# Optimization experiments

Measured on AMD Instinct MI355X. Metric: run time of the kernel, lower is better.

Reference implementation:

```python
import jax, jax.numpy as jnp
import numpy as np

LN_EPS = 1e-5
ROPE_BASE = 10000.0


def rotate_half(x):
    # x: [..., d]; split into two halves (matches einops '(j d)->j d', j=2)
    d2 = x.shape[-1] // 2
    x1, x2 = x[..., :d2], x[..., d2:]
    return jnp.concatenate((-x2, x1), axis=-1)


def rotary_pos_emb(n, head_dim, dtype=jnp.float32):
    inv_freq = 1.0 / (ROPE_BASE ** (jnp.arange(0, head_dim, 2, dtype=jnp.float32) / head_dim))
    t = jnp.arange(n, dtype=jnp.float32)
    freqs = jnp.einsum('i,j->ij', t, inv_freq)          # [n, d/2]
    return jnp.concatenate((freqs, freqs), axis=-1).astype(dtype)  # [n, d]


def apply_rotary(pos, t):
    return t * jnp.cos(pos) + rotate_half(t) * jnp.sin(pos)


def setup_inputs() -> dict:
    key = jax.random.key(0)
    ks = jax.random.split(key, 4)
    b, n, dm = 2, 4096, 2048
    x = jax.random.normal(ks[0], (b, n, dm), dtype=jnp.float32)
    wq = jax.random.normal(ks[1], (dm, dm), dtype=jnp.float32) * (dm ** -0.5)
    wk = jax.random.normal(ks[2], (dm, dm), dtype=jnp.float32) * (dm ** -0.5)
    wv = jax.random.normal(ks[3], (dm, dm), dtype=jnp.float32) * (dm ** -0.5)
    return {
        'x': x,
        'ln_gamma': jnp.ones((dm,), jnp.float32),
        'ln_beta': jnp.zeros((dm,), jnp.float32),
        'wq': wq, 'wk': wk, 'wv': wv,
        'num_heads': 16,
    }


def reference(x, ln_gamma, ln_beta, wq, wk, wv, num_heads):
    b, n, dm = x.shape
    hd = dm // num_heads
    # LayerNorm (eps=1e-5, torch default)
    mu = jnp.mean(x, axis=-1, keepdims=True)
    var = jnp.mean(jnp.square(x - mu), axis=-1, keepdims=True)
    xn = (x - mu) * jax.lax.rsqrt(var + LN_EPS) * ln_gamma + ln_beta
    # QKV projections (nn.Linear, bias=False => x @ W.T; weights stored as [out,in])
    q = jnp.einsum('bnd,ed->bne', xn, wq)
    k = jnp.einsum('bnd,ed->bne', xn, wk)
    v = jnp.einsum('bnd,ed->bne', xn, wv)
    # b n (h d) -> b h n d
    split = lambda t: t.reshape(b, n, num_heads, hd).transpose(0, 2, 1, 3)
    q, k, v = split(q), split(k), split(v)
    pos = rotary_pos_emb(n, hd, x.dtype)  # [n, hd], broadcasts over b,h
    q = apply_rotary(pos, q)
    k = apply_rotary(pos, k)
    return q, k, v
```

## Files before the change

### kernel.cpp

```cpp
#include <hip/hip_runtime.h>
#include <hip/hip_bf16.h>


typedef float f32x4 __attribute__((ext_vector_type(4)));
typedef __bf16 bf16x8 __attribute__((ext_vector_type(8)));
typedef __bf16 bf16x4 __attribute__((ext_vector_type(4)));

#define DM    2048
#define NSEQ  4096
#define NH    16
#define HD    128
#define NROWS 8192
#define MAT_ELEMS (2ull*NH*NSEQ*HD)

typedef __attribute__((address_space(1))) const void GV;
typedef __attribute__((address_space(3))) void LV;
__device__ __forceinline__ void gload_lds16(const void* g, void* l) {
    __builtin_amdgcn_global_load_lds((GV*)g, (LV*)l, 16, 0, 0);
}

__global__ __launch_bounds__(256)
void ln_kernel(const float* __restrict__ x, const float* __restrict__ g,
               const float* __restrict__ be, __bf16* __restrict__ xnb) {
    int row = blockIdx.x;
    int tid = threadIdx.x;
    const float4* xr = (const float4*)(x + (size_t)row * DM);
    float4 v0 = xr[tid];
    float4 v1 = xr[tid + 256];
    float s  = v0.x + v0.y + v0.z + v0.w + v1.x + v1.y + v1.z + v1.w;
    float ss = v0.x*v0.x + v0.y*v0.y + v0.z*v0.z + v0.w*v0.w
             + v1.x*v1.x + v1.y*v1.y + v1.z*v1.z + v1.w*v1.w;
#pragma unroll
    for (int o = 32; o > 0; o >>= 1) {
        s  += __shfl_down(s, o);
        ss += __shfl_down(ss, o);
    }
    __shared__ float red[10];
    int wave = tid >> 6, lane = tid & 63;
    if (lane == 0) { red[wave] = s; red[4 + wave] = ss; }
    __syncthreads();
    if (tid == 0) {
        float S  = red[0] + red[1] + red[2] + red[3];
        float SS = red[4] + red[5] + red[6] + red[7];
        float mu  = S * (1.0f / DM);
        float var = SS * (1.0f / DM) - mu * mu;
        red[8] = mu;
        red[9] = rsqrtf(var + 1e-5f);
    }
    __syncthreads();
    float mu = red[8], rs = red[9];

    const float4* gp = (const float4*)g;
    const float4* bp = (const float4*)be;
    bf16x4* orow = (bf16x4*)(xnb + (size_t)row * DM);
    {
        float4 g0 = gp[tid], b0 = bp[tid];
        bf16x4 o;
        o[0] = (__bf16)((v0.x - mu) * rs * g0.x + b0.x);
        o[1] = (__bf16)((v0.y - mu) * rs * g0.y + b0.y);
        o[2] = (__bf16)((v0.z - mu) * rs * g0.z + b0.z);
        o[3] = (__bf16)((v0.w - mu) * rs * g0.w + b0.w);
        orow[tid] = o;
    }
    {
        float4 g1 = gp[tid + 256], b1 = bp[tid + 256];
        bf16x4 o;
        o[0] = (__bf16)((v1.x - mu) * rs * g1.x + b1.x);
        o[1] = (__bf16)((v1.y - mu) * rs * g1.y + b1.y);
        o[2] = (__bf16)((v1.z - mu) * rs * g1.z + b1.z);
        o[3] = (__bf16)((v1.w - mu) * rs * g1.w + b1.w);
        orow[tid + 256] = o;
    }
}

__global__ __launch_bounds__(256)
void cvt3_kernel(const float* __restrict__ a0, const float* __restrict__ a1,
                 const float* __restrict__ a2, __bf16* __restrict__ o) {
    int bid = blockIdx.x;
    const float* a = (bid < 2048) ? a0 : (bid < 4096) ? a1 : a2;
    size_t base = ((size_t)(bid & 2047) * 256 + threadIdx.x) * 8;
    float4 v0 = *(const float4*)(a + base);
    float4 v1 = *(const float4*)(a + base + 4);
    bf16x8 r;
    r[0] = (__bf16)v0.x; r[1] = (__bf16)v0.y; r[2] = (__bf16)v0.z; r[3] = (__bf16)v0.w;
    r[4] = (__bf16)v1.x; r[5] = (__bf16)v1.y; r[6] = (__bf16)v1.z; r[7] = (__bf16)v1.w;
    *(bf16x8*)(o + (size_t)(bid >> 11) * 4194304 + base) = r;
}


__device__ __forceinline__ void loadA(bf16x8 (&a)[4], const __bf16* Sp,
                                      int base, int oo) {
#pragma unroll
    for (int mi = 0; mi < 4; mi++)
        a[mi] = *(const bf16x8*)(Sp + base + mi * 1024 + oo);
}
__device__ __forceinline__ void loadB(bf16x8 (&b)[4], const __bf16* Sp,
                                      int base, int oo) {
#pragma unroll
    for (int j = 0; j < 4; j++)
        b[j] = *(const bf16x8*)(Sp + base + (j * 16 + (j >> 1) * 32) * 64 + oo);
}

template<int RB>
__device__ __forceinline__ void cluster(f32x4 (&acc)[8][4], bf16x8 (&a)[4],
                                        bf16x8 (&b)[4]) {
    __builtin_amdgcn_s_setprio(1);
#pragma unroll
    for (int mi = 0; mi < 4; mi++)
#pragma unroll
        for (int ni = 0; ni < 4; ni++)
            acc[RB + mi][ni] = __builtin_amdgcn_mfma_f32_16x16x32_bf16(
                a[mi], b[ni], acc[RB + mi][ni], 0, 0, 0);
    __builtin_amdgcn_s_setprio(0);
}

#define FENCE asm volatile("" ::: "memory")
#define BAR   do { FENCE; __builtin_amdgcn_s_barrier(); FENCE; } while (0)
#define VM8   asm volatile("s_waitcnt vmcnt(8)" ::: "memory")
#define VM6   asm volatile("s_waitcnt vmcnt(6)" ::: "memory")
#define VM2   asm volatile("s_waitcnt vmcnt(2)" ::: "memory")
#define VM0   asm volatile("s_waitcnt vmcnt(0)" ::: "memory")
#define VMX   do {} while (0)

#define STGA(P, kt, HF) do { \
    gload_lds16(pA + (size_t)((HF) * 64 + w * 8) * DM + (kt) * 64,       &As[P][((HF) * 8 + w) * 512]); \
    gload_lds16(pA + (size_t)((HF) * 64 + 128 + w * 8) * DM + (kt) * 64, &As[P][((HF) * 8 + 16 + w) * 512]); \
} while (0)
#define STGB(P, kt, HF) do { \
    gload_lds16(pB + (size_t)((HF) * 64 + w * 8) * DM + (kt) * 64,       &Bs[P][((HF) * 8 + w) * 512]); \
    gload_lds16(pB + (size_t)((HF) * 64 + 128 + w * 8) * DM + (kt) * 64, &Bs[P][((HF) * 8 + 16 + w) * 512]); \
} while (0)

#define KTILE(kt, P, Q, SG0, SG2, SG3, W0, W2) do { \
     \
    loadA(a0, &As[P][0], baseA, o0); \
    loadB(b0, &Bs[P][0], baseB, o0); \
    if (SG0) STGA(Q, (kt) + 1, 1); \
    W0; BAR; cluster<0>(acc, a0, b0); BAR; \
     \
    loadA(a1, &As[P][0], baseA, o1); \
    loadB(b1, &Bs[P][0], baseB, o1); \
    BAR; cluster<0>(acc, a1, b1); BAR; \
     \
    loadA(a0, &As[P][0], baseA + 4096, o0); \
    if (SG2) { STGA(P, (kt) + 2, 0); STGB(P, (kt) + 2, 0); } \
    W2; BAR; cluster<4>(acc, a0, b0); BAR; \
     \
    loadA(a1, &As[P][0], baseA + 4096, o1); \
    if (SG3) STGB(P, (kt) + 2, 1); \
    BAR; cluster<4>(acc, a1, b1); BAR; \
} while (0)

__global__ __launch_bounds__(512, 2)
void gemm_qkv(const __bf16* __restrict__ A,
              const __bf16* __restrict__ Wq,
              const __bf16* __restrict__ Wk,
              const __bf16* __restrict__ Wv,
              float* __restrict__ out) {
    __shared__ __bf16 As[2][16384];
    __shared__ __bf16 Bs[2][16384];

    int tid = threadIdx.x;
    int w = tid >> 6, l = tid & 63;
    int wm = w >> 2, wn = w & 3;

    int bid = blockIdx.x;
    int x = bid & 7;
    int ridx = bid >> 3;
    int q = ridx >> 5;
    int s = ridx & 31;
    int mtp, ntp;
    if (q == 0)      { mtp = s >> 3;       ntp = s & 7; }
    else if (q == 1) { mtp = 4 + (s >> 3); ntp = s & 7; }
    else             { mtp = s & 7;        ntp = 8 + (s >> 3); }
    int mt = (x & 3) * 8 + mtp;
    int nt = (x >> 2) * 12 + ntp;
    int mat = nt >> 3, ntb = nt & 7;
    const __bf16* Wp = (mat == 0) ? Wq : (mat == 1) ? Wk : Wv;
    int row0 = mt * 256, colp = ntb * 256;

    int lr = l >> 3;
    int lco = ((l & 7) ^ lr) * 8;
    const __bf16* pA = A  + (size_t)(row0 + lr) * DM + lco;
    const __bf16* pB = Wp + (size_t)(colp + lr) * DM + lco;

    int baseA = (wm * 128 + (l & 15)) * 64;
    int baseB = ((wn & 1) * 32 + (wn >> 1) * 128 + (l & 15)) * 64;
    int o0 = ((l >> 4) * 8) ^ ((l & 7) * 8);
    int o1 = o0 ^ 32;

    STGA(0, 0, 0); STGB(0, 0, 0); STGB(0, 0, 1); STGA(0, 0, 1);
    STGA(1, 1, 0); STGB(1, 1, 0); STGB(1, 1, 1);

    f32x4 acc[8][4];
#pragma unroll
    for (int i = 0; i < 8; i++)
#pragma unroll
        for (int j = 0; j < 4; j++)
            acc[i][j] = (f32x4){0.f, 0.f, 0.f, 0.f};

    bf16x8 a0[4], a1[4], b0[4], b1[4];

    VM8;
    BAR;

#pragma unroll 1
    for (int kt = 0; kt < 30; kt += 2) {
        KTILE(kt,     0, 1, 1, 1, 1, VM8, VM6);
        KTILE(kt + 1, 1, 0, 1, 1, 1, VM8, VM6);
    }
    KTILE(30, 0, 1, 1, 0, 0, VM8, VM2);
    KTILE(31, 1, 0, 0, 0, 0, VM0, VMX);

    float* op = out + (size_t)mat * MAT_ELEMS;
    int hd_lo = (wn & 1) * 32 + (l & 15);
    int head = ntb * 2 + (wn >> 1);
    int r_base = row0 + wm * 128 + ((l >> 4) << 2);
    float if0 = exp2f(-0.20762051f * (float)hd_lo);
    float if1 = exp2f(-0.20762051f * (float)(hd_lo + 16));

    if (mat < 2) {
#pragma unroll
        for (int mi = 0; mi < 8; mi++) {
#pragma unroll
            for (int j = 0; j < 4; j++) {
                int r = r_base + mi * 16 + j;
                int b = r >> 12, n = r & 4095;
                float fn = (float)n;
                float* rowp = op + ((size_t)((b * NH + head) * NSEQ + n)) * HD;
#pragma unroll
                for (int ni = 0; ni < 2; ni++) {
                    float lo = acc[mi][ni][j], hi = acc[mi][ni + 2][j];
                    float sv, cv;
                    __sincosf(fn * (ni ? if1 : if0), &sv, &cv);
                    rowp[hd_lo + ni * 16]      = lo * cv - hi * sv;
                    rowp[hd_lo + ni * 16 + 64] = hi * cv + lo * sv;
                }
            }
        }
    } else {
#pragma unroll
        for (int mi = 0; mi < 8; mi++) {
#pragma unroll
            for (int j = 0; j < 4; j++) {
                int r = r_base + mi * 16 + j;
                int b = r >> 12, n = r & 4095;
                float* rowp = op + ((size_t)((b * NH + head) * NSEQ + n)) * HD;
#pragma unroll
                for (int ni = 0; ni < 2; ni++) {
                    rowp[hd_lo + ni * 16]      = acc[mi][ni][j];
                    rowp[hd_lo + ni * 16 + 64] = acc[mi][ni + 2][j];
                }
            }
        }
    }
}

extern "C" void kernel_launch(void* const* d_in, const int* in_sizes, int n_in,
                              void* d_out, int out_size, void* d_ws, size_t ws_size,
                              hipStream_t stream) {
    const float* x  = (const float*)d_in[0];
    const float* g  = (const float*)d_in[1];
    const float* be = (const float*)d_in[2];
    const float* wq = (const float*)d_in[3];
    const float* wk = (const float*)d_in[4];
    const float* wv = (const float*)d_in[5];
    float* out = (float*)d_out;

    char* ws = (char*)d_ws;
    __bf16* xnb = (__bf16*)ws;
    __bf16* wb  = (__bf16*)(ws + 33554432);

    ln_kernel<<<NROWS, 256, 0, stream>>>(x, g, be, xnb);
    cvt3_kernel<<<6144, 256, 0, stream>>>(wq, wk, wv, wb);
    gemm_qkv<<<768, 512, 0, stream>>>(xnb, wb, wb + 4194304, wb + 8388608, out);
}
```

Before: 233.8 us.

## Merge K sub-steps into two phases per tile with doubled fragment loads

Restructures each 64-wide K tile of the QKV GEMM from four LDS-load/MFMA phases into two. Each phase loads both K halves of the A and B fragments at once and issues 32 MFMAs back to back. This halves the number of barriers per tile and regroups the global-to-LDS prefetch stages, with the vmcnt waits retuned to match. The cost is more live fragment registers, which may hurt occupancy at 2 waves per SIMD, and a coarser overlap between LDS loads and MFMA issue.

```diff
diff --git a/kernel.cpp b/kernel.cpp
--- a/kernel.cpp
+++ b/kernel.cpp
@@ -88,37 +88,44 @@
 }
 
 
-__device__ __forceinline__ void loadA(bf16x8 (&a)[4], const __bf16* Sp,
-                                      int base, int oo) {
+__device__ __forceinline__ void loadA2(bf16x8 (&a)[4][2], const __bf16* Sp,
+                                       int base, int o0, int o1) {
+#pragma unroll
+    for (int mi = 0; mi < 4; mi++) {
+        a[mi][0] = *(const bf16x8*)(Sp + base + mi * 1024 + o0);
+        a[mi][1] = *(const bf16x8*)(Sp + base + mi * 1024 + o1);
+    }
+}
+__device__ __forceinline__ void loadB2(bf16x8 (&b)[4][2], const __bf16* Sp,
+                                       int base, int o0, int o1) {
+#pragma unroll
+    for (int j = 0; j < 4; j++) {
+        int ro = (j * 16 + (j >> 1) * 32) * 64;
+        b[j][0] = *(const bf16x8*)(Sp + base + ro + o0);
+        b[j][1] = *(const bf16x8*)(Sp + base + ro + o1);
+    }
+}
+
+template<int RB>
+__device__ __forceinline__ void cluster32(f32x4 (&acc)[8][4], bf16x8 (&a)[4][2],
+                                          bf16x8 (&b)[4][2]) {
+    __builtin_amdgcn_s_setprio(1);
 #pragma unroll
     for (int mi = 0; mi < 4; mi++)
-        a[mi] = *(const bf16x8*)(Sp + base + mi * 1024 + oo);
-}
-__device__ __forceinline__ void loadB(bf16x8 (&b)[4], const __bf16* Sp,
-                                      int base, int oo) {
-#pragma unroll
-    for (int j = 0; j < 4; j++)
-        b[j] = *(const bf16x8*)(Sp + base + (j * 16 + (j >> 1) * 32) * 64 + oo);
-}
-
-template<int RB>
-__device__ __forceinline__ void cluster(f32x4 (&acc)[8][4], bf16x8 (&a)[4],
-                                        bf16x8 (&b)[4]) {
-    __builtin_amdgcn_s_setprio(1);
-#pragma unroll
-    for (int mi = 0; mi < 4; mi++)
-#pragma unroll
-        for (int ni = 0; ni < 4; ni++)
+#pragma unroll
+        for (int ni = 0; ni < 4; ni++) {
             acc[RB + mi][ni] = __builtin_amdgcn_mfma_f32_16x16x32_bf16(
-                a[mi], b[ni], acc[RB + mi][ni], 0, 0, 0);
+                a[mi][0], b[ni][0], acc[RB + mi][ni], 0, 0, 0);
+            acc[RB + mi][ni] = __builtin_amdgcn_mfma_f32_16x16x32_bf16(
+                a[mi][1], b[ni][1], acc[RB + mi][ni], 0, 0, 0);
+        }
     __builtin_amdgcn_s_setprio(0);
 }
 
 #define FENCE asm volatile("" ::: "memory")
 #define BAR   do { FENCE; __builtin_amdgcn_s_barrier(); FENCE; } while (0)
 #define VM8   asm volatile("s_waitcnt vmcnt(8)" ::: "memory")
-#define VM6   asm volatile("s_waitcnt vmcnt(6)" ::: "memory")
-#define VM2   asm volatile("s_waitcnt vmcnt(2)" ::: "memory")
+#define VM4   asm volatile("s_waitcnt vmcnt(4)" ::: "memory")
 #define VM0   asm volatile("s_waitcnt vmcnt(0)" ::: "memory")
 #define VMX   do {} while (0)
 
@@ -131,24 +138,16 @@
     gload_lds16(pB + (size_t)((HF) * 64 + 128 + w * 8) * DM + (kt) * 64, &Bs[P][((HF) * 8 + 16 + w) * 512]); \
 } while (0)
 
-#define KTILE(kt, P, Q, SG0, SG2, SG3, W0, W2) do { \
+#define KT2(kt, P, Q, SGA, SGB, WA, WB) do { \
      \
-    loadA(a0, &As[P][0], baseA, o0); \
-    loadB(b0, &Bs[P][0], baseB, o0); \
-    if (SG0) STGA(Q, (kt) + 1, 1); \
-    W0; BAR; cluster<0>(acc, a0, b0); BAR; \
+    loadA2(a, &As[P][0], baseA, o0, o1); \
+    loadB2(b, &Bs[P][0], baseB, o0, o1); \
+    if (SGA) { STGA(Q, (kt) + 1, 1); STGB(Q, (kt) + 1, 1); } \
+    WA; BAR; cluster32<0>(acc, a, b); BAR; \
      \
-    loadA(a1, &As[P][0], baseA, o1); \
-    loadB(b1, &Bs[P][0], baseB, o1); \
-    BAR; cluster<0>(acc, a1, b1); BAR; \
-     \
-    loadA(a0, &As[P][0], baseA + 4096, o0); \
-    if (SG2) { STGA(P, (kt) + 2, 0); STGB(P, (kt) + 2, 0); } \
-    W2; BAR; cluster<4>(acc, a0, b0); BAR; \
-     \
-    loadA(a1, &As[P][0], baseA + 4096, o1); \
-    if (SG3) STGB(P, (kt) + 2, 1); \
-    BAR; cluster<4>(acc, a1, b1); BAR; \
+    loadA2(a, &As[P][0], baseA + 4096, o0, o1); \
+    if (SGB) { STGA(P, (kt) + 2, 0); STGB(P, (kt) + 2, 0); } \
+    WB; BAR; cluster32<4>(acc, a, b); BAR; \
 } while (0)
 
 __global__ __launch_bounds__(512, 2)
@@ -189,8 +188,9 @@
     int o0 = ((l >> 4) * 8) ^ ((l & 7) * 8);
     int o1 = o0 ^ 32;
 
-    STGA(0, 0, 0); STGB(0, 0, 0); STGB(0, 0, 1); STGA(0, 0, 1);
-    STGA(1, 1, 0); STGB(1, 1, 0); STGB(1, 1, 1);
+    STGA(0, 0, 0); STGB(0, 0, 0);
+    STGA(0, 0, 1); STGB(0, 0, 1);
+    STGA(1, 1, 0); STGB(1, 1, 0);
 
     f32x4 acc[8][4];
 #pragma unroll
@@ -199,18 +199,18 @@
         for (int j = 0; j < 4; j++)
             acc[i][j] = (f32x4){0.f, 0.f, 0.f, 0.f};
 
-    bf16x8 a0[4], a1[4], b0[4], b1[4];
-
-    VM8;
+    bf16x8 a[4][2], b[4][2];
+
+    VM4;
     BAR;
 
 #pragma unroll 1
     for (int kt = 0; kt < 30; kt += 2) {
-        KTILE(kt,     0, 1, 1, 1, 1, VM8, VM6);
-        KTILE(kt + 1, 1, 0, 1, 1, 1, VM8, VM6);
-    }
-    KTILE(30, 0, 1, 1, 0, 0, VM8, VM2);
-    KTILE(31, 1, 0, 0, 0, 0, VM0, VMX);
+        KT2(kt,     0, 1, 1, 1, VM8, VM4);
+        KT2(kt + 1, 1, 0, 1, 1, VM8, VM4);
+    }
+    KT2(30, 0, 1, 1, 0, VM8, VM0);
+    KT2(31, 1, 0, 0, 0, VMX, VMX);
 
     float* op = out + (size_t)mat * MAT_ELEMS;
     int hd_lo = (wn & 1) * 32 + (l & 15);
@@ -225,9 +225,9 @@
 #pragma unroll
             for (int j = 0; j < 4; j++) {
                 int r = r_base + mi * 16 + j;
-                int b = r >> 12, n = r & 4095;
+                int b2 = r >> 12, n = r & 4095;
                 float fn = (float)n;
-                float* rowp = op + ((size_t)((b * NH + head) * NSEQ + n)) * HD;
+                float* rowp = op + ((size_t)((b2 * NH + head) * NSEQ + n)) * HD;
 #pragma unroll
                 for (int ni = 0; ni < 2; ni++) {
                     float lo = acc[mi][ni][j], hi = acc[mi][ni + 2][j];
@@ -244,8 +244,8 @@
 #pragma unroll
             for (int j = 0; j < 4; j++) {
                 int r = r_base + mi * 16 + j;
-                int b = r >> 12, n = r & 4095;
-                float* rowp = op + ((size_t)((b * NH + head) * NSEQ + n)) * HD;
+                int b2 = r >> 12, n = r & 4095;
+                float* rowp = op + ((size_t)((b2 * NH + head) * NSEQ + n)) * HD;
 #pragma unroll
                 for (int ni = 0; ni < 2; ni++) {
                     rowp[hd_lo + ni * 16]      = acc[mi][ni][j];
```

New measurement: 231.3 us. Within noise of the previous version (-1.1%).
